# Kernel optimization log

Measured on AMD Instinct MI355X. Metric: run time of the kernel, lower is better.

## Reference

```python
import jax, jax.numpy as jnp
import numpy as np

NUM_HEADS = 8
KEY_DIM = 16
D = 32          # attn_ratio * key_dim
DH = D * NUM_HEADS  # 256
NH_KD = KEY_DIM * NUM_HEADS  # 128
DIM = 256


def _conv1x1_bn(x, W, s, b):
    # 1x1 conv (no bias) followed by eval-mode BatchNorm folded to affine.
    # x: [B, Cin, H, W], W: [Cout, Cin], s/b: [Cout]
    y = jnp.einsum('oc,bchw->bohw', W, x)
    return y * s[None, :, None, None] + b[None, :, None, None]


def setup_inputs() -> dict:
    key = jax.random.key(0)
    ks = jax.random.split(key, 16)
    B, C, H, Wd = 2, DIM, 64, 64
    rgb = jax.random.normal(ks[0], (B, C, H, Wd), dtype=jnp.float32)
    edge = jax.random.normal(ks[1], (B, C, H, Wd), dtype=jnp.float32)

    def conv_w(k, o, i):
        return jax.random.normal(k, (o, i), dtype=jnp.float32) * (1.0 / np.sqrt(i))

    def bn(k, c):
        k1, k2 = jax.random.split(k)
        s = jax.random.uniform(k1, (c,), dtype=jnp.float32, minval=0.5, maxval=1.5)
        b = jax.random.normal(k2, (c,), dtype=jnp.float32) * 0.1
        return s, b

    Wq = conv_w(ks[2], NH_KD, C); sq, bq = bn(ks[3], NH_KD)
    Wk = conv_w(ks[4], NH_KD, C); sk, bk = bn(ks[5], NH_KD)
    Wv = conv_w(ks[6], DH, C);   sv, bv = bn(ks[7], DH)
    Wp = conv_w(ks[8], C, DH);   sp, bp = bn(ks[9], C)
    return dict(rgb=rgb, edge=edge, Wq=Wq, sq=sq, bq=bq, Wk=Wk, sk=sk, bk=bk,
                Wv=Wv, sv=sv, bv=bv, Wp=Wp, sp=sp, bp=bp)


def reference(rgb, edge, Wq, sq, bq, Wk, sk, bk, Wv, sv, bv, Wp, sp, bp):
    B, C, H, Wd = rgb.shape
    N = H * Wd
    # Q from rgb, K/V from edge (all 1x1 conv + BN)
    qq = _conv1x1_bn(rgb, Wq, sq, bq).reshape(B, NUM_HEADS, KEY_DIM, N)
    qq = jnp.transpose(qq, (0, 1, 3, 2))                       # [B,h,N,kd]
    kk = _conv1x1_bn(edge, Wk, sk, bk).reshape(B, NUM_HEADS, KEY_DIM, N)  # [B,h,kd,N]
    vv = _conv1x1_bn(edge, Wv, sv, bv).reshape(B, NUM_HEADS, D, N)
    vv = jnp.transpose(vv, (0, 1, 3, 2))                       # [B,h,N,d]
    # NOTE: original forward does NOT apply self.scale -- faithful omission.
    attn = jnp.einsum('bhnk,bhkm->bhnm', qq, kk)               # [B,h,N,N]
    attn = jax.nn.softmax(attn, axis=-1)
    xx = jnp.einsum('bhnm,bhmd->bhnd', attn, vv)               # [B,h,N,d]
    xx = jnp.transpose(xx, (0, 1, 3, 2)).reshape(B, DH, H, Wd)
    xx = jax.nn.relu(xx)                                       # activation before proj conv
    xx = _conv1x1_bn(xx, Wp, sp, bp)                           # [B,C,H,W]
    return xx
```

## Files before the change

kernel.cpp:

```cpp
#include <hip/hip_runtime.h>
#include <hip/hip_bf16.h>

#define NB 2
#define CIN 256
#define NPIX 4096
#define NHEADS 8
#define KD 16
#define DV 32
#define DH 256
#define NHKD 128

typedef short bf16x8 __attribute__((ext_vector_type(8)));
typedef short s16x4 __attribute__((ext_vector_type(4)));
typedef float f32x4 __attribute__((ext_vector_type(4)));
typedef float f32x16 __attribute__((ext_vector_type(16)));
typedef unsigned int u32x2 __attribute__((ext_vector_type(2)));
typedef unsigned int u32x4 __attribute__((ext_vector_type(4)));

#define LOG2E 1.4426950408889634f

static __device__ __forceinline__ unsigned short f2bf(float f) {
    __hip_bfloat16 h = __float2bfloat16(f);
    return __builtin_bit_cast(unsigned short, h);
}

__global__ __launch_bounds__(256) void k_prep(
    const float* __restrict__ Wq, const float* __restrict__ Wk,
    const float* __restrict__ Wv, const float* __restrict__ Wp,
    unsigned short* __restrict__ wq, unsigned short* __restrict__ wk,
    unsigned short* __restrict__ wv, unsigned short* __restrict__ wp)
{
    int i = blockIdx.x * 256 + threadIdx.x;
    if (i < NHKD * CIN) { wq[i] = f2bf(Wq[i]); wk[i] = f2bf(Wk[i]); }
    if (i < DH * CIN)   { wv[i] = f2bf(Wv[i]); wp[i] = f2bf(Wp[i]); }
}

__global__ __launch_bounds__(256) void k_qkv(
    const float* __restrict__ rgb, const float* __restrict__ edge,
    const unsigned short* __restrict__ wq, const unsigned short* __restrict__ wk,
    const unsigned short* __restrict__ wv,
    const float* __restrict__ sq, const float* __restrict__ bq,
    const float* __restrict__ sk, const float* __restrict__ bk,
    const float* __restrict__ sv, const float* __restrict__ bv,
    unsigned short* __restrict__ Qw, unsigned short* __restrict__ Kw,
    unsigned short* __restrict__ Vw)
{
    const int nb = blockIdx.x;
    const int ob = blockIdx.y;
    const int b  = blockIdx.z;
    const int tid = threadIdx.x;
    const int wave = tid >> 6, lane = tid & 63;
    const int cl = lane & 15, g = lane >> 4;

    const float* X; const unsigned short* W; const float* sc; const float* bi;
    int obase, job;
    if (ob < 2)      { X = rgb  + (size_t)b*CIN*NPIX; W = wq; sc = sq; bi = bq; obase = ob*64;     job = 0; }
    else if (ob < 4) { X = edge + (size_t)b*CIN*NPIX; W = wk; sc = sk; bi = bk; obase = (ob-2)*64; job = 1; }
    else             { X = edge + (size_t)b*CIN*NPIX; W = wv; sc = sv; bi = bv; obase = (ob-4)*64; job = 2; }

    __shared__ float xt[32 * 65];

    f32x4 acc[4];
    #pragma unroll
    for (int i = 0; i < 4; i++) acc[i] = (f32x4)0.f;

    const int n0 = nb * 64;
    const int ow = obase + wave * 16 + cl;
    const unsigned short* Wrow = W + (size_t)ow * CIN;

    for (int kt = 0; kt < 8; kt++) {
        __syncthreads();
        {
            int tr = tid >> 6;
            int tc = tid & 63;
            #pragma unroll
            for (int r = 0; r < 8; r++) {
                int c_local = r * 4 + tr;
                xt[c_local * 65 + tc] = X[(size_t)(kt * 32 + c_local) * NPIX + n0 + tc];
            }
        }
        __syncthreads();
        #pragma unroll
        for (int ns = 0; ns < 4; ns++) {
            bf16x8 a;
            #pragma unroll
            for (int j = 0; j < 8; j++)
                a[j] = (short)f2bf(xt[(8 * g + j) * 65 + ns * 16 + cl]);
            bf16x8 wfrag = *reinterpret_cast<const bf16x8*>(Wrow + kt * 32 + 8 * g);
            acc[ns] = __builtin_amdgcn_mfma_f32_16x16x32_bf16(a, wfrag, acc[ns], 0, 0, 0);
        }
    }

    const float sco = sc[ow], bio = bi[ow];
    if (job == 2) {
        int h = ow >> 5, d = ow & 31;
        unsigned short* dst = Vw + ((size_t)((b * 8 + h) * 32 + d)) * NPIX;
        #pragma unroll
        for (int ns = 0; ns < 4; ns++) {
            int nr = n0 + ns * 16 + 4 * g;
            s16x4 pk;
            #pragma unroll
            for (int r = 0; r < 4; r++) pk[r] = (short)f2bf(acc[ns][r] * sco + bio);
            *reinterpret_cast<s16x4*>(dst + nr) = pk;
        }
    } else {
        float scq = sco, biq = bio;
        if (job == 0) { scq *= LOG2E; biq *= LOG2E; }
        unsigned short* base = (job == 0) ? Qw : Kw;
        int h = ow >> 4, kd = ow & 15;
        unsigned short* dst = base + ((size_t)(b * 8 + h) * NPIX) * KD + kd;
        #pragma unroll
        for (int ns = 0; ns < 4; ns++)
            #pragma unroll
            for (int r = 0; r < 4; r++) {
                int nr = n0 + ns * 16 + 4 * g + r;
                dst[(size_t)nr * KD] = f2bf(acc[ns][r] * scq + biq);
            }
    }
}

typedef const unsigned int __attribute__((address_space(1)))* gp_t;
typedef unsigned int __attribute__((address_space(3)))* lp_t;

__global__ __launch_bounds__(256) void k_attn(
    const unsigned short* __restrict__ Qw, const unsigned short* __restrict__ Kw,
    const unsigned short* __restrict__ Vw, unsigned short* __restrict__ Ow)
{
    const int qb = blockIdx.x;
    const int bh = blockIdx.y;
    const int tid = threadIdx.x;
    const int wave = tid >> 6, lane = tid & 63;
    const int l31 = lane & 31, hi = lane >> 5;

    __shared__ unsigned short Vlds[2][2048];

    const unsigned short* Kbase = Kw + (size_t)bh * NPIX * KD;
    const unsigned short* Vbase = Vw + (size_t)bh * DV * NPIX;

    const int q0 = qb * 128 + wave * 32;
    const bf16x8 qf = *(const bf16x8*)(Qw + ((size_t)bh * NPIX + q0 + l31) * KD + 8 * hi);

    const unsigned short* Kln = Kbase + (size_t)l31 * KD + 8 * hi;
#define KF0(T) (*(const bf16x8*)(Kln + ((T) * 64 + 0) * KD))
#define KF1(T) (*(const bf16x8*)(Kln + ((T) * 64 + 32) * KD))

    const int sd  = wave * 8 + (lane >> 3);
    const int scb = ((lane & 7) * 16) ^ ((sd & 7) << 4);
    const unsigned short* Vsrc = Vbase + (size_t)sd * NPIX + (scb >> 1);
#define STAGE(T, BUF) __builtin_amdgcn_global_load_lds( \
        (gp_t)(const void*)(Vsrc + (size_t)(T) * 64),    \
        (lp_t)(void*)(&Vlds[BUF][wave * 512]), 16, 0, 0)

    const int vsw = (l31 & 7) << 4;

    f32x16 o = (f32x16)0.f;
    float l_run = 0.f;
    const f32x16 z16 = (f32x16)0.f;

    bf16x8 kfa0, kfa1, kfb0, kfb1;
    STAGE(0, 0);
    kfa0 = KF0(0); kfa1 = KF1(0);

#define TILE_BODY(T, KA0, KA1, CUR, KB0, KB1) do {                               \
    __syncthreads();                                                             \
    if ((T) + 1 < 64) {                                                          \
        STAGE((T) + 1, 1 - (CUR));                                               \
        KB0 = KF0((T) + 1);                                                      \
        KB1 = KF1((T) + 1);                                                      \
    }                                                                            \
    f32x16 s0 = __builtin_amdgcn_mfma_f32_32x32x16_bf16(KA0, qf, z16, 0, 0, 0);  \
    f32x16 s1 = __builtin_amdgcn_mfma_f32_32x32x16_bf16(KA1, qf, z16, 0, 0, 0);  \
    _Pragma("unroll") for (int i = 0; i < 16; ++i)                               \
        s0[i] = __builtin_amdgcn_exp2f(s0[i]);                                   \
    _Pragma("unroll") for (int i = 0; i < 16; ++i)                               \
        s1[i] = __builtin_amdgcn_exp2f(s1[i]);                                   \
    float t[16];                                                                 \
    _Pragma("unroll") for (int i = 0; i < 16; ++i) t[i] = s0[i] + s1[i];         \
    _Pragma("unroll") for (int i = 0; i < 8; ++i) t[i] += t[i + 8];              \
    _Pragma("unroll") for (int i = 0; i < 4; ++i) t[i] += t[i + 4];              \
    t[0] += t[2]; t[1] += t[3]; t[0] += t[1];                                    \
    l_run += t[0];                                                               \
    unsigned up[16];                                                             \
    _Pragma("unroll") for (int ss = 0; ss < 8; ++ss) {                           \
        up[ss]     = (unsigned)f2bf(s0[2*ss]) | ((unsigned)f2bf(s0[2*ss+1]) << 16); \
        up[8 + ss] = (unsigned)f2bf(s1[2*ss]) | ((unsigned)f2bf(s1[2*ss+1]) << 16); } \
    _Pragma("unroll") for (int gg = 0; gg < 4; ++gg) {                           \
        u32x2 r0 = __builtin_amdgcn_permlane32_swap(up[4*gg+0], up[4*gg+2],      \
                                                    false, false);               \
        up[4*gg+0] = r0.x; up[4*gg+2] = r0.y;                                    \
        u32x2 r1 = __builtin_amdgcn_permlane32_swap(up[4*gg+1], up[4*gg+3],      \
                                                    false, false);               \
        up[4*gg+1] = r1.x; up[4*gg+3] = r1.y; }                                  \
    _Pragma("unroll") for (int c = 0; c < 4; ++c) {                              \
        u32x4 av;                                                                \
        av.x = up[4*c + 0];                                                      \
        av.y = up[4*c + 1];                                                      \
        av.z = up[4*c + 2];                                                      \
        av.w = up[4*c + 3];                                                      \
        const int vidx = (l31 * 128 + ((32 * c + 16 * hi) ^ vsw)) >> 1;          \
        bf16x8 vb = *(const bf16x8*)(&Vlds[CUR][vidx]);                          \
        o = __builtin_amdgcn_mfma_f32_32x32x16_bf16(                             \
                __builtin_bit_cast(bf16x8, av), vb, o, 0, 0, 0);                 \
    }                                                                            \
} while (0)

    for (int tt = 0; tt < 32; ++tt) {
        TILE_BODY(2 * tt,     kfa0, kfa1, 0, kfb0, kfb1);
        TILE_BODY(2 * tt + 1, kfb0, kfb1, 1, kfa0, kfa1);
    }

    l_run += __shfl_xor(l_run, 32, 64);

    const float linv = __builtin_amdgcn_rcpf(l_run);
    const int b = bh >> 3, h = bh & 7;
    #pragma unroll
    for (int r = 0; r < 16; ++r) {
        const int qr = (r & 3) + 8 * (r >> 2) + 4 * hi;
        const float lr = __shfl(linv, qr, 64);
        const float v = fmaxf(o[r] * lr, 0.f);
        Ow[((size_t)b * NPIX + q0 + qr) * DH + h * DV + l31] = f2bf(v);
    }
#undef TILE_BODY
#undef STAGE
#undef KF0
#undef KF1
}

__global__ __launch_bounds__(256) void k_proj(
    const unsigned short* __restrict__ Xo, const unsigned short* __restrict__ wp,
    const float* __restrict__ sp, const float* __restrict__ bp,
    float* __restrict__ out)
{
    const int nb = blockIdx.x;
    const int b  = blockIdx.y;
    const int tid = threadIdx.x;
    const int wave = tid >> 6, lane = tid & 63;
    const int cl = lane & 15, g = lane >> 4;

    const int cbase = wave * 64;
    f32x4 acc[4][4];
    #pragma unroll
    for (int i = 0; i < 4; i++)
        #pragma unroll
        for (int j = 0; j < 4; j++) acc[i][j] = (f32x4)0.f;

    const unsigned short* Xb = Xo + ((size_t)b * NPIX + nb * 64) * DH;

    #pragma unroll
    for (int kt = 0; kt < 8; kt++) {
        bf16x8 afr[4];
        #pragma unroll
        for (int cs = 0; cs < 4; cs++)
            afr[cs] = *reinterpret_cast<const bf16x8*>(wp + (size_t)(cbase + cs * 16 + cl) * DH + kt * 32 + 8 * g);
        #pragma unroll
        for (int ns = 0; ns < 4; ns++) {
            bf16x8 bfr = *reinterpret_cast<const bf16x8*>(Xb + (size_t)(ns * 16 + cl) * DH + kt * 32 + 8 * g);
            #pragma unroll
            for (int cs = 0; cs < 4; cs++)
                acc[cs][ns] = __builtin_amdgcn_mfma_f32_16x16x32_bf16(afr[cs], bfr, acc[cs][ns], 0, 0, 0);
        }
    }

    #pragma unroll
    for (int cs = 0; cs < 4; cs++)
        #pragma unroll
        for (int r = 0; r < 4; r++) {
            int c = cbase + cs * 16 + 4 * g + r;
            float scv = sp[c], biv = bp[c];
            float* dst = out + ((size_t)b * DH + c) * NPIX + nb * 64;
            #pragma unroll
            for (int ns = 0; ns < 4; ns++)
                dst[ns * 16 + cl] = acc[cs][ns][r] * scv + biv;
        }
}

extern "C" void kernel_launch(void* const* d_in, const int* in_sizes, int n_in,
                              void* d_out, int out_size, void* d_ws, size_t ws_size,
                              hipStream_t stream) {
    const float* rgb  = (const float*)d_in[0];
    const float* edge = (const float*)d_in[1];
    const float* Wq = (const float*)d_in[2];
    const float* sq = (const float*)d_in[3];
    const float* bq = (const float*)d_in[4];
    const float* Wk = (const float*)d_in[5];
    const float* sk = (const float*)d_in[6];
    const float* bk = (const float*)d_in[7];
    const float* Wv = (const float*)d_in[8];
    const float* sv = (const float*)d_in[9];
    const float* bv = (const float*)d_in[10];
    const float* Wp = (const float*)d_in[11];
    const float* sp = (const float*)d_in[12];
    const float* bp = (const float*)d_in[13];
    float* out = (float*)d_out;

    char* ws = (char*)d_ws;
    unsigned short* wq = (unsigned short*)(ws + 0);
    unsigned short* wk = (unsigned short*)(ws + (64 << 10));
    unsigned short* wv = (unsigned short*)(ws + (128 << 10));
    unsigned short* wp = (unsigned short*)(ws + (256 << 10));
    size_t o = 384 << 10;
    unsigned short* Qw = (unsigned short*)(ws + o); o += (size_t)16 * NPIX * KD * 2;
    unsigned short* Kw = (unsigned short*)(ws + o); o += (size_t)16 * NPIX * KD * 2;
    unsigned short* Vw = (unsigned short*)(ws + o); o += (size_t)16 * DV * NPIX * 2;
    unsigned short* Ow = (unsigned short*)(ws + o);

    k_prep<<<dim3(256), dim3(256), 0, stream>>>(Wq, Wk, Wv, Wp, wq, wk, wv, wp);
    k_qkv<<<dim3(64, 8, NB), dim3(256), 0, stream>>>(rgb, edge, wq, wk, wv,
                                                     sq, bq, sk, bk, sv, bv, Qw, Kw, Vw);
    k_attn<<<dim3(32, 16), dim3(256), 0, stream>>>(Qw, Kw, Vw, Ow);
    k_proj<<<dim3(64, NB), dim3(256), 0, stream>>>(Ow, wp, sp, bp, out);
}
```

Measured before the change: 106.3 us.

## Split attention keys across waves with cross-wave LDS reduction

Each block now handles 32 queries, and its four waves each take a quarter of the key/value sequence instead of the full sequence. Partial outputs and row sums are reduced through shared memory before normalisation, ReLU and a vectorised store. The grid grows from 512 to 2048 blocks to raise parallelism and drop per-tile block barriers. In exchange, each wave loads its own V tiles without double buffering (it waits on vmcnt(0) every tile), and every block re-reads K/V, which raises redundant K/V traffic fourfold.

```diff
diff --git a/kernel.cpp b/kernel.cpp
--- a/kernel.cpp
+++ b/kernel.cpp
@@ -126,30 +126,30 @@
     const unsigned short* __restrict__ Qw, const unsigned short* __restrict__ Kw,
     const unsigned short* __restrict__ Vw, unsigned short* __restrict__ Ow)
 {
-    const int qb = blockIdx.x;
+    const int qg = blockIdx.x;
     const int bh = blockIdx.y;
     const int tid = threadIdx.x;
     const int wave = tid >> 6, lane = tid & 63;
     const int l31 = lane & 31, hi = lane >> 5;
 
-    __shared__ unsigned short Vlds[2][2048];
+    __shared__ union {
+        unsigned short v[4][2048];
+        float o[4][32][32];
+    } sh;
+    __shared__ float shl[4][32];
 
     const unsigned short* Kbase = Kw + (size_t)bh * NPIX * KD;
     const unsigned short* Vbase = Vw + (size_t)bh * DV * NPIX;
 
-    const int q0 = qb * 128 + wave * 32;
+    const int q0 = qg * 32;
     const bf16x8 qf = *(const bf16x8*)(Qw + ((size_t)bh * NPIX + q0 + l31) * KD + 8 * hi);
 
     const unsigned short* Kln = Kbase + (size_t)l31 * KD + 8 * hi;
 #define KF0(T) (*(const bf16x8*)(Kln + ((T) * 64 + 0) * KD))
 #define KF1(T) (*(const bf16x8*)(Kln + ((T) * 64 + 32) * KD))
 
-    const int sd  = wave * 8 + (lane >> 3);
-    const int scb = ((lane & 7) * 16) ^ ((sd & 7) << 4);
-    const unsigned short* Vsrc = Vbase + (size_t)sd * NPIX + (scb >> 1);
-#define STAGE(T, BUF) __builtin_amdgcn_global_load_lds( \
-        (gp_t)(const void*)(Vsrc + (size_t)(T) * 64),    \
-        (lp_t)(void*)(&Vlds[BUF][wave * 512]), 16, 0, 0)
+    const int scb = ((lane & 7) * 16) ^ ((lane >> 3) << 4);
+    const unsigned short* Vln = Vbase + (size_t)(lane >> 3) * NPIX + (scb >> 1);
 
     const int vsw = (l31 & 7) << 4;
 
@@ -157,73 +157,89 @@
     float l_run = 0.f;
     const f32x16 z16 = (f32x16)0.f;
 
-    bf16x8 kfa0, kfa1, kfb0, kfb1;
-    STAGE(0, 0);
-    kfa0 = KF0(0); kfa1 = KF1(0);
-
-#define TILE_BODY(T, KA0, KA1, CUR, KB0, KB1) do {                               \
-    __syncthreads();                                                             \
-    if ((T) + 1 < 64) {                                                          \
-        STAGE((T) + 1, 1 - (CUR));                                               \
-        KB0 = KF0((T) + 1);                                                      \
-        KB1 = KF1((T) + 1);                                                      \
-    }                                                                            \
-    f32x16 s0 = __builtin_amdgcn_mfma_f32_32x32x16_bf16(KA0, qf, z16, 0, 0, 0);  \
-    f32x16 s1 = __builtin_amdgcn_mfma_f32_32x32x16_bf16(KA1, qf, z16, 0, 0, 0);  \
-    _Pragma("unroll") for (int i = 0; i < 16; ++i)                               \
-        s0[i] = __builtin_amdgcn_exp2f(s0[i]);                                   \
-    _Pragma("unroll") for (int i = 0; i < 16; ++i)                               \
-        s1[i] = __builtin_amdgcn_exp2f(s1[i]);                                   \
-    float t[16];                                                                 \
-    _Pragma("unroll") for (int i = 0; i < 16; ++i) t[i] = s0[i] + s1[i];         \
-    _Pragma("unroll") for (int i = 0; i < 8; ++i) t[i] += t[i + 8];              \
-    _Pragma("unroll") for (int i = 0; i < 4; ++i) t[i] += t[i + 4];              \
-    t[0] += t[2]; t[1] += t[3]; t[0] += t[1];                                    \
-    l_run += t[0];                                                               \
-    unsigned up[16];                                                             \
-    _Pragma("unroll") for (int ss = 0; ss < 8; ++ss) {                           \
-        up[ss]     = (unsigned)f2bf(s0[2*ss]) | ((unsigned)f2bf(s0[2*ss+1]) << 16); \
-        up[8 + ss] = (unsigned)f2bf(s1[2*ss]) | ((unsigned)f2bf(s1[2*ss+1]) << 16); } \
-    _Pragma("unroll") for (int gg = 0; gg < 4; ++gg) {                           \
-        u32x2 r0 = __builtin_amdgcn_permlane32_swap(up[4*gg+0], up[4*gg+2],      \
-                                                    false, false);               \
-        up[4*gg+0] = r0.x; up[4*gg+2] = r0.y;                                    \
-        u32x2 r1 = __builtin_amdgcn_permlane32_swap(up[4*gg+1], up[4*gg+3],      \
-                                                    false, false);               \
-        up[4*gg+1] = r1.x; up[4*gg+3] = r1.y; }                                  \
-    _Pragma("unroll") for (int c = 0; c < 4; ++c) {                              \
-        u32x4 av;                                                                \
-        av.x = up[4*c + 0];                                                      \
-        av.y = up[4*c + 1];                                                      \
-        av.z = up[4*c + 2];                                                      \
-        av.w = up[4*c + 3];                                                      \
-        const int vidx = (l31 * 128 + ((32 * c + 16 * hi) ^ vsw)) >> 1;          \
-        bf16x8 vb = *(const bf16x8*)(&Vlds[CUR][vidx]);                          \
-        o = __builtin_amdgcn_mfma_f32_32x32x16_bf16(                             \
-                __builtin_bit_cast(bf16x8, av), vb, o, 0, 0, 0);                 \
-    }                                                                            \
-} while (0)
-
-    for (int tt = 0; tt < 32; ++tt) {
-        TILE_BODY(2 * tt,     kfa0, kfa1, 0, kfb0, kfb1);
-        TILE_BODY(2 * tt + 1, kfb0, kfb1, 1, kfa0, kfa1);
-    }
+    for (int t = 0; t < 16; ++t) {
+        const int T = wave * 16 + t;
+        bf16x8 ka0 = KF0(T);
+        bf16x8 ka1 = KF1(T);
+        #pragma unroll
+        for (int j = 0; j < 4; ++j)
+            __builtin_amdgcn_global_load_lds(
+                (gp_t)(const void*)(Vln + (size_t)j * 8 * NPIX + T * 64),
+                (lp_t)(void*)(&sh.v[wave][j * 512]), 16, 0, 0);
+
+        f32x16 s0 = __builtin_amdgcn_mfma_f32_32x32x16_bf16(ka0, qf, z16, 0, 0, 0);
+        f32x16 s1 = __builtin_amdgcn_mfma_f32_32x32x16_bf16(ka1, qf, z16, 0, 0, 0);
+        #pragma unroll
+        for (int i = 0; i < 16; ++i) s0[i] = __builtin_amdgcn_exp2f(s0[i]);
+        #pragma unroll
+        for (int i = 0; i < 16; ++i) s1[i] = __builtin_amdgcn_exp2f(s1[i]);
+
+        float t16[16];
+        #pragma unroll
+        for (int i = 0; i < 16; ++i) t16[i] = s0[i] + s1[i];
+        #pragma unroll
+        for (int i = 0; i < 8; ++i) t16[i] += t16[i + 8];
+        #pragma unroll
+        for (int i = 0; i < 4; ++i) t16[i] += t16[i + 4];
+        t16[0] += t16[2]; t16[1] += t16[3];
+        l_run += t16[0] + t16[1];
+
+        unsigned up[16];
+        #pragma unroll
+        for (int ss = 0; ss < 8; ++ss) {
+            up[ss]     = (unsigned)f2bf(s0[2*ss]) | ((unsigned)f2bf(s0[2*ss+1]) << 16);
+            up[8 + ss] = (unsigned)f2bf(s1[2*ss]) | ((unsigned)f2bf(s1[2*ss+1]) << 16);
+        }
+        #pragma unroll
+        for (int gg = 0; gg < 4; ++gg) {
+            u32x2 r0 = __builtin_amdgcn_permlane32_swap(up[4*gg+0], up[4*gg+2], false, false);
+            up[4*gg+0] = r0.x; up[4*gg+2] = r0.y;
+            u32x2 r1 = __builtin_amdgcn_permlane32_swap(up[4*gg+1], up[4*gg+3], false, false);
+            up[4*gg+1] = r1.x; up[4*gg+3] = r1.y;
+        }
+
+        asm volatile("s_waitcnt vmcnt(0)" ::: "memory");
+        #pragma unroll
+        for (int c = 0; c < 4; ++c) {
+            u32x4 av;
+            av.x = up[4*c + 0];
+            av.y = up[4*c + 1];
+            av.z = up[4*c + 2];
+            av.w = up[4*c + 3];
+            const int vidx = wave * 2048 + ((l31 * 128 + ((32 * c + 16 * hi) ^ vsw)) >> 1);
+            bf16x8 vb = *(const bf16x8*)(&sh.v[0][vidx]);
+            o = __builtin_amdgcn_mfma_f32_32x32x16_bf16(
+                    __builtin_bit_cast(bf16x8, av), vb, o, 0, 0, 0);
+        }
+    }
+#undef KF0
+#undef KF1
 
     l_run += __shfl_xor(l_run, 32, 64);
 
-    const float linv = __builtin_amdgcn_rcpf(l_run);
-    const int b = bh >> 3, h = bh & 7;
     #pragma unroll
     for (int r = 0; r < 16; ++r) {
         const int qr = (r & 3) + 8 * (r >> 2) + 4 * hi;
-        const float lr = __shfl(linv, qr, 64);
-        const float v = fmaxf(o[r] * lr, 0.f);
-        Ow[((size_t)b * NPIX + q0 + qr) * DH + h * DV + l31] = f2bf(v);
-    }
-#undef TILE_BODY
-#undef STAGE
-#undef KF0
-#undef KF1
+        sh.o[wave][qr][l31] = o[r];
+    }
+    if (hi == 0) shl[wave][l31] = l_run;
+    __syncthreads();
+
+    const int q = tid >> 3;
+    const int d0 = (tid & 7) * 4;
+    const float lsum = shl[0][q] + shl[1][q] + shl[2][q] + shl[3][q];
+    const float linv = __builtin_amdgcn_rcpf(lsum);
+    float v[4];
+    #pragma unroll
+    for (int i = 0; i < 4; ++i) {
+        float s = sh.o[0][q][d0+i] + sh.o[1][q][d0+i] + sh.o[2][q][d0+i] + sh.o[3][q][d0+i];
+        v[i] = fmaxf(s * linv, 0.f);
+    }
+    const int b = bh >> 3, h = bh & 7;
+    u32x2 pk;
+    pk.x = (unsigned)f2bf(v[0]) | ((unsigned)f2bf(v[1]) << 16);
+    pk.y = (unsigned)f2bf(v[2]) | ((unsigned)f2bf(v[3]) << 16);
+    *reinterpret_cast<u32x2*>(Ow + ((size_t)b * NPIX + q0 + q) * DH + h * DV + d0) = pk;
 }
 
 __global__ __launch_bounds__(256) void k_proj(
@@ -307,6 +323,6 @@
     k_prep<<<dim3(256), dim3(256), 0, stream>>>(Wq, Wk, Wv, Wp, wq, wk, wv, wp);
     k_qkv<<<dim3(64, 8, NB), dim3(256), 0, stream>>>(rgb, edge, wq, wk, wv,
                                                      sq, bq, sk, bk, sv, bv, Qw, Kw, Vw);
-    k_attn<<<dim3(32, 16), dim3(256), 0, stream>>>(Qw, Kw, Vw, Ow);
+    k_attn<<<dim3(128, 16), dim3(256), 0, stream>>>(Qw, Kw, Vw, Ow);
     k_proj<<<dim3(64, NB), dim3(256), 0, stream>>>(Ow, wp, sp, bp, out);
 }
```

New measurement: 95.67 us. 10.0% less time.
